# Performance work log

Measured on AMD Instinct MI355X. Metric: run time of the kernel, lower is better.

## Reference

```python
import jax, jax.numpy as jnp
import numpy as np

EPS = 1e-9

def setup_inputs() -> dict:
    key = jax.random.key(0)
    k1, k2 = jax.random.split(key)
    N, K, D = 65536, 512, 768
    return {
        "embeddings": jax.random.normal(k1, (N, D), dtype=jnp.float32),
        "cluster_centers": jax.random.normal(k2, (K, D), dtype=jnp.float32),
        "alpha": 1.0,
    }


def reference(embeddings, cluster_centers, alpha):
    # Student-t soft assignment (DEC): q_ik = (1 + ||x_i - c_k||^2 / alpha)^(-(alpha+1)/2), row-normalized.
    # Squared distance via expansion to avoid materializing the [N, K, D] broadcast:
    x_sq = jnp.sum(embeddings * embeddings, axis=1, keepdims=True)          # [N, 1]
    c_sq = jnp.sum(cluster_centers * cluster_centers, axis=1)               # [K]
    cross = jnp.einsum("nd,kd->nk", embeddings, cluster_centers)            # [N, K]
    norm_squared = jnp.maximum(x_sq - 2.0 * cross + c_sq[None, :], 0.0)     # [N, K]
    numerator = 1.0 / (1.0 + norm_squared / alpha)
    power = (alpha + 1.0) / 2.0
    numerator = numerator ** power
    cluster_p = numerator / jnp.sum(numerator, axis=1, keepdims=True)       # [N, K]
    return cluster_p
```

## Files before the change

### kernel.cpp

```cpp
#include <hip/hip_runtime.h>
#include <hip/hip_bf16.h>

#define D_DIM 768
#define K_CL  512
#define BM    64
#define BK    32
#define NSTEP 24

using f32x4 = __attribute__((ext_vector_type(4))) float;
using s16x8 = __attribute__((ext_vector_type(8))) short;
using u16x8 = __attribute__((ext_vector_type(8))) unsigned short;
using u16x4 = __attribute__((ext_vector_type(4))) unsigned short;

static __device__ __forceinline__ unsigned short f2bf(float f) {
    __hip_bfloat16 h = __float2bfloat16(f);
    unsigned short u;
    __builtin_memcpy(&u, &h, 2);
    return u;
}

__global__ void prep_centers_kernel(const float* __restrict__ C,
                                    unsigned short* __restrict__ Cbws,
                                    float* __restrict__ csq) {
    const int r = blockIdx.x;
    const int l = threadIdx.x;
    const float* src = C + (size_t)r * D_DIM;
    float sq = 0.f;
#pragma unroll
    for (int jj = 0; jj < 2; ++jj) {
        const int j = l + jj * 64;
        if (j < 96) {
            const int t = j >> 2, s = j & 3;
            const int k0 = t * 32 + s * 8;
            f32x4 v0 = *reinterpret_cast<const f32x4*>(src + k0);
            f32x4 v1 = *reinterpret_cast<const f32x4*>(src + k0 + 4);
            u16x8 b;
            b[0] = f2bf(v0[0]); b[1] = f2bf(v0[1]); b[2] = f2bf(v0[2]); b[3] = f2bf(v0[3]);
            b[4] = f2bf(v1[0]); b[5] = f2bf(v1[1]); b[6] = f2bf(v1[2]); b[7] = f2bf(v1[3]);
            sq += v0[0]*v0[0] + v0[1]*v0[1] + v0[2]*v0[2] + v0[3]*v0[3]
                + v1[0]*v1[0] + v1[1]*v1[1] + v1[2]*v1[2] + v1[3]*v1[3];
            const int g = t * 2048 + (r >> 6) * 256 + ((r >> 4) & 3) * 64
                        + s * 16 + (r & 15);
            *reinterpret_cast<u16x8*>(Cbws + (size_t)g * 8) = b;
        }
    }
#pragma unroll
    for (int m = 1; m < 64; m <<= 1) sq += __shfl_xor(sq, m, 64);
    if (l == 0) csq[r] = sq;
}

__global__ __launch_bounds__(512, 4) void dec_main_kernel(
    const float* __restrict__ X,
    const unsigned short* __restrict__ Cbws,
    const float* __restrict__ csq,
    const float* __restrict__ alpha_ptr,
    float* __restrict__ out)
{
    __shared__ unsigned short Al[2][BM * BK];
    __shared__ float part[8][BM];
    __shared__ float xsql[BM];
    __shared__ float invl[BM];

    const int tid  = threadIdx.x;
    const int lane = tid & 63;
    const int wn   = tid >> 6;
    const int m0   = blockIdx.x * BM;

    const int arow  = tid >> 3;
    const int acol8 = tid & 7;
    const float* aptr = X + (size_t)(m0 + arow) * D_DIM + acol8 * 4;
    const int awbyte = arow * 64
                     + ((((acol8 >> 1) ^ ((arow >> 1) & 3))) << 4)
                     + (acol8 & 1) * 8;

    const int fr = lane & 15;
    const int fg = lane >> 4;
    const int abase = fr * 64 + ((fg ^ ((fr >> 1) & 3)) << 4);

    const unsigned short* bptr = Cbws + (size_t)(wn * 256 + lane) * 8;

    f32x4 acc[4][4] = {};
    s16x8 bA[4];
    float sqp = 0.f;

    f32x4 areg = *reinterpret_cast<const f32x4*>(aptr);
#pragma unroll
    for (int nf = 0; nf < 4; ++nf)
        bA[nf] = *reinterpret_cast<const s16x8*>(bptr + nf * 512);
    {
        u16x4 ab;
        ab[0] = f2bf(areg[0]); ab[1] = f2bf(areg[1]);
        ab[2] = f2bf(areg[2]); ab[3] = f2bf(areg[3]);
        sqp += areg[0]*areg[0] + areg[1]*areg[1] + areg[2]*areg[2] + areg[3]*areg[3];
        *reinterpret_cast<u16x4*>((char*)&Al[0][0] + awbyte) = ab;
    }
    areg = *reinterpret_cast<const f32x4*>(aptr + BK);
    asm volatile("s_waitcnt lgkmcnt(0)" ::: "memory");
    __builtin_amdgcn_sched_barrier(0);
    __builtin_amdgcn_s_barrier();

    for (int t = 0; t < NSTEP; ++t) {
        {
            const char* ab = (const char*)&Al[t & 1][0] + abase;
            s16x8 afr[4];
#pragma unroll
            for (int mf = 0; mf < 4; ++mf)
                afr[mf] = *reinterpret_cast<const s16x8*>(ab + mf * 1024);
            __builtin_amdgcn_s_setprio(1);
#pragma unroll
            for (int nf = 0; nf < 4; ++nf) {
#pragma unroll
                for (int mf = 0; mf < 4; ++mf)
                    acc[mf][nf] = __builtin_amdgcn_mfma_f32_16x16x32_bf16(
                        afr[mf], bA[nf], acc[mf][nf], 0, 0, 0);
            }
            __builtin_amdgcn_s_setprio(0);
        }
        if (t + 1 < NSTEP) {
            const unsigned short* bp = bptr + (size_t)(t + 1) * 16384;
#pragma unroll
            for (int nf = 0; nf < 4; ++nf)
                bA[nf] = *reinterpret_cast<const s16x8*>(bp + nf * 512);
            u16x4 ab;
            ab[0] = f2bf(areg[0]); ab[1] = f2bf(areg[1]);
            ab[2] = f2bf(areg[2]); ab[3] = f2bf(areg[3]);
            sqp += areg[0]*areg[0] + areg[1]*areg[1] + areg[2]*areg[2] + areg[3]*areg[3];
            *reinterpret_cast<u16x4*>((char*)&Al[(t + 1) & 1][0] + awbyte) = ab;
            if (t + 2 < NSTEP)
                areg = *reinterpret_cast<const f32x4*>(aptr + (t + 2) * BK);
            asm volatile("s_waitcnt lgkmcnt(0)" ::: "memory");
            __builtin_amdgcn_sched_barrier(0);
            __builtin_amdgcn_s_barrier();
        }
    }

    sqp += __shfl_xor(sqp, 1, 64);
    sqp += __shfl_xor(sqp, 2, 64);
    sqp += __shfl_xor(sqp, 4, 64);
    if ((tid & 7) == 0) xsql[arow] = sqp;
    __syncthreads();

    const float alpha     = alpha_ptr[0];
    const float inv_alpha = 1.0f / alpha;
    const float power     = 0.5f * (alpha + 1.0f);
    const bool  p1        = (power == 1.0f);

    float csqr[4];
#pragma unroll
    for (int nf = 0; nf < 4; ++nf)
        csqr[nf] = csq[wn * 64 + nf * 16 + fr];

#pragma unroll
    for (int mf = 0; mf < 4; ++mf) {
#pragma unroll
        for (int j = 0; j < 4; ++j) {
            const int rloc = mf * 16 + fg * 4 + j;
            const float xs = xsql[rloc];
            float rp = 0.f;
#pragma unroll
            for (int nf = 0; nf < 4; ++nf) {
                float d2 = xs + csqr[nf] - 2.0f * acc[mf][nf][j];
                d2 = fmaxf(d2, 0.0f);
                const float base = 1.0f + d2 * inv_alpha;
                const float nm = p1 ? (1.0f / base)
                                    : exp2f(-power * log2f(base));
                acc[mf][nf][j] = nm;
                rp += nm;
            }
#pragma unroll
            for (int m = 1; m < 16; m <<= 1) rp += __shfl_xor(rp, m, 64);
            if (fr == 0) part[wn][rloc] = rp;
        }
    }
    __syncthreads();
    if (tid < BM) {
        float s = 0.f;
#pragma unroll
        for (int w = 0; w < 8; ++w) s += part[w][tid];
        invl[tid] = 1.0f / s;
    }
    __syncthreads();

#pragma unroll
    for (int mf = 0; mf < 4; ++mf) {
#pragma unroll
        for (int j = 0; j < 4; ++j) {
            const int rloc = mf * 16 + fg * 4 + j;
            const float iv = invl[rloc];
            float* orow = out + (size_t)(m0 + rloc) * K_CL + wn * 64 + fr;
#pragma unroll
            for (int nf = 0; nf < 4; ++nf)
                orow[nf * 16] = acc[mf][nf][j] * iv;
        }
    }
}

extern "C" void kernel_launch(void* const* d_in, const int* in_sizes, int n_in,
                              void* d_out, int out_size, void* d_ws, size_t ws_size,
                              hipStream_t stream) {
    const float* X     = (const float*)d_in[0];
    const float* C     = (const float*)d_in[1];
    const float* alpha = (const float*)d_in[2];
    float* out = (float*)d_out;
    const int N = in_sizes[0] / D_DIM;

    unsigned short* Cbws = (unsigned short*)d_ws;
    float* csq = (float*)((char*)d_ws + (size_t)K_CL * D_DIM * sizeof(unsigned short));

    prep_centers_kernel<<<K_CL, 64, 0, stream>>>(C, Cbws, csq);
    dec_main_kernel<<<N / BM, 512, 0, stream>>>(X, Cbws, csq, alpha, out);
}
```

Baseline: 119.7 us.

## Double row tile to 128 with 16-wave blocks to reuse center fragments

Doubles the per-block row tile from 64 to 128 and launches 1024 threads, arranged as 2 waves along rows by 8 along clusters. Each center tile fetched from global memory is now reused across twice as many rows, halving redundant L2 reads of the bf16 centers. The epilogue is also split into separate alpha==1 and general-power branches, removing a per-element select. The risk is that 1024-thread blocks with a request for 4 blocks per CU can raise register pressure and reduce scheduling flexibility.

```diff
diff --git a/kernel.cpp b/kernel.cpp
--- a/kernel.cpp
+++ b/kernel.cpp
@@ -3,7 +3,7 @@
 
 #define D_DIM 768
 #define K_CL  512
-#define BM    64
+#define BM    128
 #define BK    32
 #define NSTEP 24
 
@@ -49,7 +49,7 @@
     if (l == 0) csq[r] = sq;
 }
 
-__global__ __launch_bounds__(512, 4) void dec_main_kernel(
+__global__ __launch_bounds__(1024, 4) void dec_main_kernel(
     const float* __restrict__ X,
     const unsigned short* __restrict__ Cbws,
     const float* __restrict__ csq,
@@ -63,7 +63,9 @@
 
     const int tid  = threadIdx.x;
     const int lane = tid & 63;
-    const int wn   = tid >> 6;
+    const int wid  = tid >> 6;
+    const int wm   = wid >> 3;
+    const int wn   = wid & 7;
     const int m0   = blockIdx.x * BM;
 
     const int arow  = tid >> 3;
@@ -75,7 +77,7 @@
 
     const int fr = lane & 15;
     const int fg = lane >> 4;
-    const int abase = fr * 64 + ((fg ^ ((fr >> 1) & 3)) << 4);
+    const int abase = wm * 4096 + fr * 64 + ((fg ^ ((fr >> 1) & 3)) << 4);
 
     const unsigned short* bptr = Cbws + (size_t)(wn * 256 + lane) * 8;
 
@@ -150,26 +152,48 @@
     for (int nf = 0; nf < 4; ++nf)
         csqr[nf] = csq[wn * 64 + nf * 16 + fr];
 
-#pragma unroll
-    for (int mf = 0; mf < 4; ++mf) {
-#pragma unroll
-        for (int j = 0; j < 4; ++j) {
-            const int rloc = mf * 16 + fg * 4 + j;
-            const float xs = xsql[rloc];
-            float rp = 0.f;
-#pragma unroll
-            for (int nf = 0; nf < 4; ++nf) {
-                float d2 = xs + csqr[nf] - 2.0f * acc[mf][nf][j];
-                d2 = fmaxf(d2, 0.0f);
-                const float base = 1.0f + d2 * inv_alpha;
-                const float nm = p1 ? (1.0f / base)
-                                    : exp2f(-power * log2f(base));
-                acc[mf][nf][j] = nm;
-                rp += nm;
+    if (p1) {
+#pragma unroll
+        for (int mf = 0; mf < 4; ++mf) {
+#pragma unroll
+            for (int j = 0; j < 4; ++j) {
+                const int rloc = wm * 64 + mf * 16 + fg * 4 + j;
+                const float xs = xsql[rloc];
+                float rp = 0.f;
+#pragma unroll
+                for (int nf = 0; nf < 4; ++nf) {
+                    float d2 = xs + csqr[nf] - 2.0f * acc[mf][nf][j];
+                    d2 = fmaxf(d2, 0.0f);
+                    const float nm = 1.0f / (1.0f + d2 * inv_alpha);
+                    acc[mf][nf][j] = nm;
+                    rp += nm;
+                }
+#pragma unroll
+                for (int m = 1; m < 16; m <<= 1) rp += __shfl_xor(rp, m, 64);
+                if (fr == 0) part[wn][rloc] = rp;
             }
-#pragma unroll
-            for (int m = 1; m < 16; m <<= 1) rp += __shfl_xor(rp, m, 64);
-            if (fr == 0) part[wn][rloc] = rp;
+        }
+    } else {
+#pragma unroll
+        for (int mf = 0; mf < 4; ++mf) {
+#pragma unroll
+            for (int j = 0; j < 4; ++j) {
+                const int rloc = wm * 64 + mf * 16 + fg * 4 + j;
+                const float xs = xsql[rloc];
+                float rp = 0.f;
+#pragma unroll
+                for (int nf = 0; nf < 4; ++nf) {
+                    float d2 = xs + csqr[nf] - 2.0f * acc[mf][nf][j];
+                    d2 = fmaxf(d2, 0.0f);
+                    const float base = 1.0f + d2 * inv_alpha;
+                    const float nm = exp2f(-power * log2f(base));
+                    acc[mf][nf][j] = nm;
+                    rp += nm;
+                }
+#pragma unroll
+                for (int m = 1; m < 16; m <<= 1) rp += __shfl_xor(rp, m, 64);
+                if (fr == 0) part[wn][rloc] = rp;
+            }
         }
     }
     __syncthreads();
@@ -185,7 +209,7 @@
     for (int mf = 0; mf < 4; ++mf) {
 #pragma unroll
         for (int j = 0; j < 4; ++j) {
-            const int rloc = mf * 16 + fg * 4 + j;
+            const int rloc = wm * 64 + mf * 16 + fg * 4 + j;
             const float iv = invl[rloc];
             float* orow = out + (size_t)(m0 + rloc) * K_CL + wn * 64 + fr;
 #pragma unroll
@@ -208,5 +232,5 @@
     float* csq = (float*)((char*)d_ws + (size_t)K_CL * D_DIM * sizeof(unsigned short));
 
     prep_centers_kernel<<<K_CL, 64, 0, stream>>>(C, Cbws, csq);
-    dec_main_kernel<<<N / BM, 512, 0, stream>>>(X, Cbws, csq, alpha, out);
-}
+    dec_main_kernel<<<N / BM, 1024, 0, stream>>>(X, Cbws, csq, alpha, out);
+}
```

After: 137.7 us. 1.15x slower.
